# Performance work log

Measured on AMD Instinct MI355X. Metric: run time of the kernel, lower is better.

The kernel has to match this reference:

```python
import jax, jax.numpy as jnp
import numpy as np

B, P, N, D = 32, 100, 1000, 128
SQRT_D = 11.313708498984761
CLIP = 10.0


def setup_inputs() -> dict:
    key = jax.random.key(0)
    ks = jax.random.split(key, 8)
    s = 1.0 / np.sqrt(D)  # keep k ~ N(0,1) so exp(k) is stable
    return {
        "encoded_nodes": jax.random.normal(ks[0], (B, N, D), jnp.float32),
        "encoded_q1": jax.random.normal(ks[1], (B, P, D), jnp.float32),
        "encoded_last_node": jax.random.normal(ks[2], (B, P, D), jnp.float32),
        "cur_dist": jax.random.uniform(ks[3], (B, P, N), jnp.float32),
        "ninf_mask": jnp.zeros((B, P, N), jnp.float32),
        "log_scale": jnp.ones((1,), jnp.float32),
        "Wq_first": jax.random.normal(ks[4], (D, D), jnp.float32) * s,
        "Wq_last": jax.random.normal(ks[5], (D, D), jnp.float32) * s,
        "Wk": jax.random.normal(ks[6], (D, D), jnp.float32) * s,
        "Wv": jax.random.normal(ks[7], (D, D), jnp.float32) * s,
        "dist_alpha_1": jnp.ones((1,), jnp.float32),
        "AFT_dist_alpha_1": jnp.ones((1,), jnp.float32),
    }


def reference(encoded_nodes, encoded_q1, encoded_last_node, cur_dist, ninf_mask,
              log_scale, Wq_first, Wq_last, Wk, Wv, dist_alpha_1, AFT_dist_alpha_1):
    # set_kv / set_q1 (torch Linear: x @ W.T)
    k = jnp.einsum('bnd,ed->bne', encoded_nodes, Wk)          # [B,N,D]
    v = jnp.einsum('bnd,ed->bne', encoded_nodes, Wv)          # [B,N,D]
    q_first = jnp.einsum('bpd,ed->bpe', encoded_q1, Wq_first) # [B,P,D]
    q_last = jnp.einsum('bpd,ed->bpe', encoded_last_node, Wq_last)
    q = q_first + q_last

    cur_dist_out = -cur_dist                                   # [B,P,N]
    bias_scale = log_scale * AFT_dist_alpha_1 * cur_dist_out + ninf_mask
    ebias = jnp.exp(bias_scale)                                # [B,P,N]
    ek = jnp.exp(k)                                            # [B,N,D]
    num = jnp.einsum('bpn,bnd->bpd', ebias, ek * v)
    den = jnp.einsum('bpn,bnd->bpd', ebias, ek)
    aft_out = jax.nn.sigmoid(q) * (num / den)                  # [B,P,D]

    score = jnp.einsum('bpd,bnd->bpn', aft_out, encoded_nodes) / SQRT_D
    score = score + log_scale * dist_alpha_1 * cur_dist_out
    score = CLIP * jnp.tanh(score) + ninf_mask
    return jax.nn.softmax(score, axis=2)
```

## Files before the change

### kernel.cpp

```cpp
#include <hip/hip_runtime.h>
#include <hip/hip_bf16.h>
#include <math.h>

#define B 32
#define P 100
#define N 1000
#define D 128

constexpr float SQRT_D_INV = 1.0f / 11.313708498984761f;
constexpr float CLIPV = 10.0f;

__device__ __forceinline__ void fma4(float4& a, float s, const float4& b) {
    a.x = fmaf(s, b.x, a.x);
    a.y = fmaf(s, b.y, a.y);
    a.z = fmaf(s, b.z, a.z);
    a.w = fmaf(s, b.w, a.w);
}

__global__ void transpose_w4(const float* __restrict__ Wk,
                             const float* __restrict__ Wv,
                             const float* __restrict__ Wqf,
                             const float* __restrict__ Wql,
                             float* __restrict__ wkT,
                             float* __restrict__ wvT,
                             float* __restrict__ wqfT,
                             float* __restrict__ wqlT) {
    const int e = blockIdx.x;
    const int d = threadIdx.x;
    wkT[e * D + d]  = Wk[d * D + e];
    wvT[e * D + d]  = Wv[d * D + e];
    wqfT[e * D + d] = Wqf[d * D + e];
    wqlT[e * D + d] = Wql[d * D + e];
}

#define TT 64
__global__ __launch_bounds__(256) void transpose_nodes(
        const float* __restrict__ nodes, float* __restrict__ nodesT) {
    __shared__ float sh[TT][D + 1];
    const int ntiles = (N + TT - 1) / TT;
    const int b  = blockIdx.x / ntiles;
    const int n0 = (blockIdx.x % ntiles) * TT;
    const int t = threadIdx.x;
    const int rows = min(TT, N - n0);

    const float4* src = (const float4*)(nodes + ((long)b * N + n0) * D);
    for (int i = t; i < rows * (D / 4); i += 256) {
        int r = i >> 5, c = i & 31;
        float4 v = src[(long)r * (D / 4) + c];
        sh[r][c * 4 + 0] = v.x; sh[r][c * 4 + 1] = v.y;
        sh[r][c * 4 + 2] = v.z; sh[r][c * 4 + 3] = v.w;
    }
    __syncthreads();

    const int nl = t & 63;
    const int eg = t >> 6;
    if (nl < rows) {
        #pragma unroll
        for (int k = 0; k < 32; ++k) {
            int e = eg * 32 + k;
            nodesT[((long)b * D + e) * N + n0 + nl] = sh[nl][e];
        }
    }
}

#define R1 32
__global__ __launch_bounds__(256, 2) void kv_kernel(
        const float* __restrict__ nodes,
        const float* __restrict__ wkT,
        const float* __restrict__ wvT,
        float* __restrict__ ek,
        float* __restrict__ ekv) {
    __shared__ float sh[R1][D];
    const int t = threadIdx.x;
    const int dq = t & 31;
    const int rl = t >> 5;
    const long row0 = (long)blockIdx.x * R1;

    const float4* src = (const float4*)(nodes + row0 * D);
    float4* dst = (float4*)(&sh[0][0]);
    #pragma unroll
    for (int i = 0; i < (R1 * D / 4) / 256; ++i)
        dst[t + i * 256] = src[t + i * 256];
    __syncthreads();

    float4 ka[4], va[4];
    #pragma unroll
    for (int rr = 0; rr < 4; ++rr) {
        ka[rr] = make_float4(0.f, 0.f, 0.f, 0.f);
        va[rr] = make_float4(0.f, 0.f, 0.f, 0.f);
    }

    const float* wkp = wkT + dq * 4;
    const float* wvp = wvT + dq * 4;
    #pragma unroll 4
    for (int e0 = 0; e0 < D; e0 += 4) {
        float4 wk4[4], wv4[4];
        #pragma unroll
        for (int ee = 0; ee < 4; ++ee) {
            wk4[ee] = *(const float4*)(wkp + (e0 + ee) * D);
            wv4[ee] = *(const float4*)(wvp + (e0 + ee) * D);
        }
        #pragma unroll
        for (int rr = 0; rr < 4; ++rr) {
            float4 s4 = *(const float4*)(&sh[rl * 4 + rr][e0]);
            fma4(ka[rr], s4.x, wk4[0]); fma4(ka[rr], s4.y, wk4[1]);
            fma4(ka[rr], s4.z, wk4[2]); fma4(ka[rr], s4.w, wk4[3]);
            fma4(va[rr], s4.x, wv4[0]); fma4(va[rr], s4.y, wv4[1]);
            fma4(va[rr], s4.z, wv4[2]); fma4(va[rr], s4.w, wv4[3]);
        }
    }

    #pragma unroll
    for (int rr = 0; rr < 4; ++rr) {
        long row = row0 + rl * 4 + rr;
        float4 e4;
        e4.x = __expf(ka[rr].x); e4.y = __expf(ka[rr].y);
        e4.z = __expf(ka[rr].z); e4.w = __expf(ka[rr].w);
        float4 ev;
        ev.x = e4.x * va[rr].x; ev.y = e4.y * va[rr].y;
        ev.z = e4.z * va[rr].z; ev.w = e4.w * va[rr].w;
        *(float4*)(ek + row * D + dq * 4) = e4;
        *(float4*)(ekv + row * D + dq * 4) = ev;
    }
}

#define R2 16
__global__ __launch_bounds__(256, 2) void q_kernel(
        const float* __restrict__ q1,
        const float* __restrict__ qlast,
        const float* __restrict__ wqfT,
        const float* __restrict__ wqlT,
        float* __restrict__ qsig) {
    __shared__ float sh1[R2][D];
    __shared__ float sh2[R2][D];
    const int t = threadIdx.x;
    const int dq = t & 31;
    const int rl = t >> 5;
    const long row0 = (long)blockIdx.x * R2;

    const float4* s1 = (const float4*)(q1 + row0 * D);
    const float4* s2 = (const float4*)(qlast + row0 * D);
    float4* d1 = (float4*)(&sh1[0][0]);
    float4* d2 = (float4*)(&sh2[0][0]);
    #pragma unroll
    for (int i = 0; i < (R2 * D / 4) / 256; ++i) {
        d1[t + i * 256] = s1[t + i * 256];
        d2[t + i * 256] = s2[t + i * 256];
    }
    __syncthreads();

    float4 acc[2];
    acc[0] = make_float4(0.f, 0.f, 0.f, 0.f);
    acc[1] = make_float4(0.f, 0.f, 0.f, 0.f);

    const float* wfp = wqfT + dq * 4;
    const float* wlp = wqlT + dq * 4;
    #pragma unroll 4
    for (int e0 = 0; e0 < D; e0 += 4) {
        float4 wf4[4], wl4[4];
        #pragma unroll
        for (int ee = 0; ee < 4; ++ee) {
            wf4[ee] = *(const float4*)(wfp + (e0 + ee) * D);
            wl4[ee] = *(const float4*)(wlp + (e0 + ee) * D);
        }
        #pragma unroll
        for (int rr = 0; rr < 2; ++rr) {
            float4 a4 = *(const float4*)(&sh1[rl * 2 + rr][e0]);
            float4 b4 = *(const float4*)(&sh2[rl * 2 + rr][e0]);
            fma4(acc[rr], a4.x, wf4[0]); fma4(acc[rr], a4.y, wf4[1]);
            fma4(acc[rr], a4.z, wf4[2]); fma4(acc[rr], a4.w, wf4[3]);
            fma4(acc[rr], b4.x, wl4[0]); fma4(acc[rr], b4.y, wl4[1]);
            fma4(acc[rr], b4.z, wl4[2]); fma4(acc[rr], b4.w, wl4[3]);
        }
    }

    #pragma unroll
    for (int rr = 0; rr < 2; ++rr) {
        long row = row0 + rl * 2 + rr;
        float4 s;
        s.x = 1.0f / (1.0f + __expf(-acc[rr].x));
        s.y = 1.0f / (1.0f + __expf(-acc[rr].y));
        s.z = 1.0f / (1.0f + __expf(-acc[rr].z));
        s.w = 1.0f / (1.0f + __expf(-acc[rr].w));
        *(float4*)(qsig + row * D + dq * 4) = s;
    }
}

#define PT 20
__global__ __launch_bounds__(128, 2) void aft_part_kernel(
        const float* __restrict__ cur_dist,
        const float* __restrict__ ninf,
        const float* __restrict__ ek,
        const float* __restrict__ ekv,
        const float* __restrict__ log_scale,
        const float* __restrict__ aft_alpha,
        float* __restrict__ pnum,
        float* __restrict__ pden,
        int NC, int L) {
    __shared__ float eb[128][PT];
    const int t = threadIdx.x;
    const int dq = t & 31;
    const int pl = t >> 5;
    const int c  = blockIdx.x % NC;
    const int pt = (blockIdx.x / NC) % (P / PT);
    const int b  = blockIdx.x / (NC * (P / PT));
    const int p0 = pt * PT;
    const int n_begin = c * L;
    const int n_end = min(N, n_begin + L);
    const float lsA = log_scale[0] * aft_alpha[0];

    float4 num[5], den[5];
    #pragma unroll
    for (int i = 0; i < 5; ++i) {
        num[i] = make_float4(0.f, 0.f, 0.f, 0.f);
        den[i] = make_float4(0.f, 0.f, 0.f, 0.f);
    }

    for (int n0 = n_begin; n0 < n_end; n0 += 128) {
        const int lim = min(128, n_end - n0);
        __syncthreads();
        if (t < lim) {
            int n = n0 + t;
            #pragma unroll
            for (int i = 0; i < PT; ++i) {
                long idx = ((long)b * P + p0 + i) * N + n;
                eb[t][i] = __expf(fmaf(-lsA, cur_dist[idx], ninf[idx]));
            }
        }
        __syncthreads();
        #pragma unroll 4
        for (int j = 0; j < lim; ++j) {
            long base = ((long)b * N + n0 + j) * D + dq * 4;
            float4 ekq = *(const float4*)(ek + base);
            float4 evq = *(const float4*)(ekv + base);
            float4 e4 = *(const float4*)(&eb[j][pl * 4]);
            float es = eb[j][16 + pl];
            fma4(num[0], e4.x, evq); fma4(den[0], e4.x, ekq);
            fma4(num[1], e4.y, evq); fma4(den[1], e4.y, ekq);
            fma4(num[2], e4.z, evq); fma4(den[2], e4.z, ekq);
            fma4(num[3], e4.w, evq); fma4(den[3], e4.w, ekq);
            fma4(num[4], es,   evq); fma4(den[4], es,   ekq);
        }
    }

    #pragma unroll
    for (int r = 0; r < 4; ++r) {
        int p = pl * 4 + r;
        long o = (((long)c * B + b) * P + p0 + p) * D + dq * 4;
        *(float4*)(pnum + o) = num[r];
        *(float4*)(pden + o) = den[r];
    }
    {
        int p = 16 + pl;
        long o = (((long)c * B + b) * P + p0 + p) * D + dq * 4;
        *(float4*)(pnum + o) = num[4];
        *(float4*)(pden + o) = den[4];
    }
}

__global__ void aft_reduce_kernel(const float* __restrict__ pnum,
                                  const float* __restrict__ pden,
                                  const float* __restrict__ qsig,
                                  float* __restrict__ aft,
                                  int NC) {
    const long i = (long)blockIdx.x * 256 + threadIdx.x;
    const long BPD = (long)B * P * D;
    float n = 0.f, d = 0.f;
    for (int c = 0; c < NC; ++c) {
        n += pnum[(long)c * BPD + i];
        d += pden[(long)c * BPD + i];
    }
    aft[i] = qsig[i] * n / d;
}

#define PT2 10
__global__ __launch_bounds__(512) void score_kernel(
        const float* __restrict__ aft,
        const float* __restrict__ nodesT,
        const float* __restrict__ cur_dist,
        const float* __restrict__ ninf,
        const float* __restrict__ log_scale,
        const float* __restrict__ dist_alpha,
        float* __restrict__ out) {
    __shared__ float sa[PT2][D];
    __shared__ float red[8][PT2];
    __shared__ float bmax[PT2];
    __shared__ float bsum[PT2];
    const int t = threadIdx.x;
    const int wid = t >> 6;
    const int pt = blockIdx.x % (P / PT2);
    const int b  = blockIdx.x / (P / PT2);
    const int p0 = pt * PT2;
    const float lsA = log_scale[0] * dist_alpha[0];

    {
        const float4* src = (const float4*)(aft + ((long)b * P + p0) * D);
        float4* dst = (float4*)(&sa[0][0]);
        if (t < PT2 * D / 4) dst[t] = src[t];
    }
    __syncthreads();

    const int n0 = t * 2;
    const bool act = (n0 < N);
    const int ncl = act ? n0 : 0;
    const float* ntb = nodesT + (long)b * D * N;

    float2 acc[PT2];
    #pragma unroll
    for (int i = 0; i < PT2; ++i) acc[i] = make_float2(0.f, 0.f);

    #pragma unroll 4
    for (int e0 = 0; e0 < D; e0 += 4) {
        float2 x[4];
        #pragma unroll
        for (int ee = 0; ee < 4; ++ee)
            x[ee] = *(const float2*)(ntb + (long)(e0 + ee) * N + ncl);
        #pragma unroll
        for (int i = 0; i < PT2; ++i) {
            float4 a4 = *(const float4*)(&sa[i][e0]);
            acc[i].x = fmaf(x[0].x, a4.x, acc[i].x);
            acc[i].x = fmaf(x[1].x, a4.y, acc[i].x);
            acc[i].x = fmaf(x[2].x, a4.z, acc[i].x);
            acc[i].x = fmaf(x[3].x, a4.w, acc[i].x);
            acc[i].y = fmaf(x[0].y, a4.x, acc[i].y);
            acc[i].y = fmaf(x[1].y, a4.y, acc[i].y);
            acc[i].y = fmaf(x[2].y, a4.z, acc[i].y);
            acc[i].y = fmaf(x[3].y, a4.w, acc[i].y);
        }
    }

    float2 sc[PT2];
    #pragma unroll
    for (int i = 0; i < PT2; ++i) {
        if (act) {
            long idx = ((long)b * P + p0 + i) * N + n0;
            float2 cd = *(const float2*)(cur_dist + idx);
            float2 nf = *(const float2*)(ninf + idx);
            float sx = fmaf(acc[i].x, SQRT_D_INV, -lsA * cd.x);
            float sy = fmaf(acc[i].y, SQRT_D_INV, -lsA * cd.y);
            float ax = fabsf(sx), ay = fabsf(sy);
            float rx = 1.f - 2.f / (__expf(2.f * ax) + 1.f);
            float ry = 1.f - 2.f / (__expf(2.f * ay) + 1.f);
            sc[i].x = CLIPV * copysignf(rx, sx) + nf.x;
            sc[i].y = CLIPV * copysignf(ry, sy) + nf.y;
        } else {
            sc[i].x = -INFINITY;
            sc[i].y = -INFINITY;
        }
    }

    #pragma unroll
    for (int i = 0; i < PT2; ++i) {
        float m = fmaxf(sc[i].x, sc[i].y);
        #pragma unroll
        for (int o = 1; o < 64; o <<= 1) m = fmaxf(m, __shfl_xor(m, o, 64));
        if ((t & 63) == 0) red[wid][i] = m;
    }
    __syncthreads();
    if (t < PT2) {
        float mm = red[0][t];
        #pragma unroll
        for (int w = 1; w < 8; ++w) mm = fmaxf(mm, red[w][t]);
        bmax[t] = mm;
    }
    __syncthreads();

    float2 ex[PT2];
    #pragma unroll
    for (int i = 0; i < PT2; ++i) {
        float m = bmax[i];
        ex[i].x = (sc[i].x > -1e30f) ? __expf(sc[i].x - m) : 0.f;
        ex[i].y = (sc[i].y > -1e30f) ? __expf(sc[i].y - m) : 0.f;
        float ssum = ex[i].x + ex[i].y;
        #pragma unroll
        for (int o = 1; o < 64; o <<= 1) ssum += __shfl_xor(ssum, o, 64);
        if ((t & 63) == 0) red[wid][i] = ssum;
    }
    __syncthreads();
    if (t < PT2) {
        float ss = red[0][t];
        #pragma unroll
        for (int w = 1; w < 8; ++w) ss += red[w][t];
        bsum[t] = ss;
    }
    __syncthreads();

    #pragma unroll
    for (int i = 0; i < PT2; ++i) {
        if (act) {
            float inv = 1.0f / bsum[i];
            long idx = ((long)b * P + p0 + i) * N + n0;
            *(float2*)(out + idx) = make_float2(ex[i].x * inv, ex[i].y * inv);
        }
    }
}

extern "C" void kernel_launch(void* const* d_in, const int* in_sizes, int n_in,
                              void* d_out, int out_size, void* d_ws, size_t ws_size,
                              hipStream_t stream) {
    const float* nodes      = (const float*)d_in[0];
    const float* q1         = (const float*)d_in[1];
    const float* qlast      = (const float*)d_in[2];
    const float* cur_dist   = (const float*)d_in[3];
    const float* ninf       = (const float*)d_in[4];
    const float* log_scale  = (const float*)d_in[5];
    const float* Wqf        = (const float*)d_in[6];
    const float* Wql        = (const float*)d_in[7];
    const float* Wk         = (const float*)d_in[8];
    const float* Wv         = (const float*)d_in[9];
    const float* dist_alpha = (const float*)d_in[10];
    const float* aft_alpha  = (const float*)d_in[11];
    float* out = (float*)d_out;

    const long BND = (long)B * N * D;
    const long BPD = (long)B * P * D;
    const long W2  = (long)D * D;

    float* ws     = (float*)d_ws;
    float* ek     = ws;
    float* ekv    = ek + BND;
    float* qsig   = ekv + BND;
    float* aft    = qsig + BPD;
    float* wkT    = aft + BPD;
    float* wvT    = wkT + W2;
    float* wqfT   = wvT + W2;
    float* wqlT   = wqfT + W2;
    float* nodesT = wqlT + W2;
    float* pnum   = nodesT + BND;

    long avail = (long)(ws_size / 4) - (3 * BND + 2 * BPD + 4 * W2);
    int NC = (int)(avail / (2 * BPD));
    if (NC < 1) NC = 1;
    if (NC > 16) NC = 16;
    int L = (N + NC - 1) / NC;
    float* pden = pnum + (long)NC * BPD;

    transpose_w4<<<D, D, 0, stream>>>(Wk, Wv, Wqf, Wql, wkT, wvT, wqfT, wqlT);
    transpose_nodes<<<B * ((N + TT - 1) / TT), 256, 0, stream>>>(nodes, nodesT);
    kv_kernel<<<(B * N) / R1, 256, 0, stream>>>(nodes, wkT, wvT, ek, ekv);
    q_kernel<<<(B * P) / R2, 256, 0, stream>>>(q1, qlast, wqfT, wqlT, qsig);
    aft_part_kernel<<<B * (P / PT) * NC, 128, 0, stream>>>(
        cur_dist, ninf, ek, ekv, log_scale, aft_alpha, pnum, pden, NC, L);
    aft_reduce_kernel<<<(int)(BPD / 256), 256, 0, stream>>>(pnum, pden, qsig, aft, NC);
    score_kernel<<<B * (P / PT2), 512, 0, stream>>>(
        aft, nodesT, cur_dist, ninf, log_scale, dist_alpha, out);
}
```

Baseline: 257.9 us.

## Widen AFT partial tile to 50 queries and fuse reduction into score kernel

The AFT partial kernel now processes 50 query rows per block with 320 threads (10 warps of 5 rows each). This halves how many times the ek/ekv rows are re-read per batch, and a padded shared buffer avoids bank conflicts. The separate partial-sum reduction kernel is removed: the score kernel now sums the NC partials and applies the sigmoid gate while loading its query tile, saving one launch and one intermediate buffer. The chunk count is capped at 12 instead of 16, which gives fewer blocks and less parallelism, and the score kernel's prologue does more global reads.

Result: slower. 286.0 us (+10.9%).

```diff
diff --git a/kernel.cpp b/kernel.cpp
--- a/kernel.cpp
+++ b/kernel.cpp
@@ -186,8 +186,9 @@
     }
 }
 
-#define PT 20
-__global__ __launch_bounds__(128, 2) void aft_part_kernel(
+#define PT 50
+#define EBS 51
+__global__ __launch_bounds__(320, 4) void aft_part_kernel(
         const float* __restrict__ cur_dist,
         const float* __restrict__ ninf,
         const float* __restrict__ ek,
@@ -197,7 +198,7 @@
         float* __restrict__ pnum,
         float* __restrict__ pden,
         int NC, int L) {
-    __shared__ float eb[128][PT];
+    __shared__ float eb[128 * EBS];
     const int t = threadIdx.x;
     const int dq = t & 31;
     const int pl = t >> 5;
@@ -219,12 +220,12 @@
     for (int n0 = n_begin; n0 < n_end; n0 += 128) {
         const int lim = min(128, n_end - n0);
         __syncthreads();
-        if (t < lim) {
-            int n = n0 + t;
-            #pragma unroll
-            for (int i = 0; i < PT; ++i) {
-                long idx = ((long)b * P + p0 + i) * N + n;
-                eb[t][i] = __expf(fmaf(-lsA, cur_dist[idx], ninf[idx]));
+        for (int s = t; s < PT * 128; s += 320) {
+            int nl = s & 127;
+            int pp = s >> 7;
+            if (nl < lim) {
+                long idx = ((long)b * P + p0 + pp) * N + (n0 + nl);
+                eb[nl * EBS + pp] = __expf(fmaf(-lsA, cur_dist[idx], ninf[idx]));
             }
         }
         __syncthreads();
@@ -233,55 +234,36 @@
             long base = ((long)b * N + n0 + j) * D + dq * 4;
             float4 ekq = *(const float4*)(ek + base);
             float4 evq = *(const float4*)(ekv + base);
-            float4 e4 = *(const float4*)(&eb[j][pl * 4]);
-            float es = eb[j][16 + pl];
-            fma4(num[0], e4.x, evq); fma4(den[0], e4.x, ekq);
-            fma4(num[1], e4.y, evq); fma4(den[1], e4.y, ekq);
-            fma4(num[2], e4.z, evq); fma4(den[2], e4.z, ekq);
-            fma4(num[3], e4.w, evq); fma4(den[3], e4.w, ekq);
-            fma4(num[4], es,   evq); fma4(den[4], es,   ekq);
-        }
-    }
-
-    #pragma unroll
-    for (int r = 0; r < 4; ++r) {
-        int p = pl * 4 + r;
-        long o = (((long)c * B + b) * P + p0 + p) * D + dq * 4;
+            const float* ebp = &eb[j * EBS + pl * 5];
+            #pragma unroll
+            for (int r = 0; r < 5; ++r) {
+                float e = ebp[r];
+                fma4(num[r], e, evq);
+                fma4(den[r], e, ekq);
+            }
+        }
+    }
+
+    #pragma unroll
+    for (int r = 0; r < 5; ++r) {
+        int p = p0 + pl * 5 + r;
+        long o = (((long)c * B + b) * P + p) * D + dq * 4;
         *(float4*)(pnum + o) = num[r];
         *(float4*)(pden + o) = den[r];
     }
-    {
-        int p = 16 + pl;
-        long o = (((long)c * B + b) * P + p0 + p) * D + dq * 4;
-        *(float4*)(pnum + o) = num[4];
-        *(float4*)(pden + o) = den[4];
-    }
-}
-
-__global__ void aft_reduce_kernel(const float* __restrict__ pnum,
-                                  const float* __restrict__ pden,
-                                  const float* __restrict__ qsig,
-                                  float* __restrict__ aft,
-                                  int NC) {
-    const long i = (long)blockIdx.x * 256 + threadIdx.x;
-    const long BPD = (long)B * P * D;
-    float n = 0.f, d = 0.f;
-    for (int c = 0; c < NC; ++c) {
-        n += pnum[(long)c * BPD + i];
-        d += pden[(long)c * BPD + i];
-    }
-    aft[i] = qsig[i] * n / d;
 }
 
 #define PT2 10
 __global__ __launch_bounds__(512) void score_kernel(
-        const float* __restrict__ aft,
+        const float* __restrict__ pnum,
+        const float* __restrict__ pden,
+        const float* __restrict__ qsig,
         const float* __restrict__ nodesT,
         const float* __restrict__ cur_dist,
         const float* __restrict__ ninf,
         const float* __restrict__ log_scale,
         const float* __restrict__ dist_alpha,
-        float* __restrict__ out) {
+        float* __restrict__ out, int NC) {
     __shared__ float sa[PT2][D];
     __shared__ float red[8][PT2];
     __shared__ float bmax[PT2];
@@ -292,11 +274,18 @@
     const int b  = blockIdx.x / (P / PT2);
     const int p0 = pt * PT2;
     const float lsA = log_scale[0] * dist_alpha[0];
-
-    {
-        const float4* src = (const float4*)(aft + ((long)b * P + p0) * D);
-        float4* dst = (float4*)(&sa[0][0]);
-        if (t < PT2 * D / 4) dst[t] = src[t];
+    const long BPD = (long)B * P * D;
+
+    for (int idx = t; idx < PT2 * D; idx += 512) {
+        int i = idx >> 7;
+        int d = idx & 127;
+        long o = ((long)b * P + p0 + i) * D + d;
+        float nsum = 0.f, dsum = 0.f;
+        for (int c = 0; c < NC; ++c) {
+            nsum += pnum[(long)c * BPD + o];
+            dsum += pden[(long)c * BPD + o];
+        }
+        sa[i][d] = qsig[o] * nsum / dsum;
     }
     __syncthreads();
 
@@ -420,18 +409,17 @@
     float* ek     = ws;
     float* ekv    = ek + BND;
     float* qsig   = ekv + BND;
-    float* aft    = qsig + BPD;
-    float* wkT    = aft + BPD;
+    float* wkT    = qsig + BPD;
     float* wvT    = wkT + W2;
     float* wqfT   = wvT + W2;
     float* wqlT   = wqfT + W2;
     float* nodesT = wqlT + W2;
     float* pnum   = nodesT + BND;
 
-    long avail = (long)(ws_size / 4) - (3 * BND + 2 * BPD + 4 * W2);
+    long avail = (long)(ws_size / 4) - (3 * BND + BPD + 4 * W2);
     int NC = (int)(avail / (2 * BPD));
     if (NC < 1) NC = 1;
-    if (NC > 16) NC = 16;
+    if (NC > 12) NC = 12;
     int L = (N + NC - 1) / NC;
     float* pden = pnum + (long)NC * BPD;
 
@@ -439,9 +427,8 @@
     transpose_nodes<<<B * ((N + TT - 1) / TT), 256, 0, stream>>>(nodes, nodesT);
     kv_kernel<<<(B * N) / R1, 256, 0, stream>>>(nodes, wkT, wvT, ek, ekv);
     q_kernel<<<(B * P) / R2, 256, 0, stream>>>(q1, qlast, wqfT, wqlT, qsig);
-    aft_part_kernel<<<B * (P / PT) * NC, 128, 0, stream>>>(
+    aft_part_kernel<<<B * (P / PT) * NC, 320, 0, stream>>>(
         cur_dist, ninf, ek, ekv, log_scale, aft_alpha, pnum, pden, NC, L);
-    aft_reduce_kernel<<<(int)(BPD / 256), 256, 0, stream>>>(pnum, pden, qsig, aft, NC);
     score_kernel<<<B * (P / PT2), 512, 0, stream>>>(
-        aft, nodesT, cur_dist, ninf, log_scale, dist_alpha, out);
-}
+        pnum, pden, qsig, nodesT, cur_dist, ninf, log_scale, dist_alpha, out, NC);
+}
```

## Register-prefetch operand loads in all GEMM loops and fuse AFT reduction into score

Applied to the files above, without the earlier changes.

Adds software double-buffering in registers to the kv, q, aft_part and score kernels: the next iteration's weight or ek/ekv/nodesT operands are loaded while the current FMAs run. The separate aft_reduce kernel is removed; score_kernel now sums the partial num/den across chunks and applies the sigmoid gate while filling its shared tile. This saves one launch and one round trip of the aft buffer through memory. The chunk length is rounded up to a multiple of 4 to fit the unrolled-by-4 loop, and the min-blocks launch bound is dropped, which may raise register use and lower occupancy.

Measured after the change: 258.8 us. No clear change (+0.4%).

```diff
diff --git a/kernel.cpp b/kernel.cpp
--- a/kernel.cpp
+++ b/kernel.cpp
@@ -64,7 +64,7 @@
 }
 
 #define R1 32
-__global__ __launch_bounds__(256, 2) void kv_kernel(
+__global__ __launch_bounds__(256) void kv_kernel(
         const float* __restrict__ nodes,
         const float* __restrict__ wkT,
         const float* __restrict__ wvT,
@@ -92,22 +92,33 @@
 
     const float* wkp = wkT + dq * 4;
     const float* wvp = wvT + dq * 4;
-    #pragma unroll 4
+
+    float4 cwk[4], cwv[4];
+    #pragma unroll
+    for (int ee = 0; ee < 4; ++ee) {
+        cwk[ee] = *(const float4*)(wkp + ee * D);
+        cwv[ee] = *(const float4*)(wvp + ee * D);
+    }
+
     for (int e0 = 0; e0 < D; e0 += 4) {
-        float4 wk4[4], wv4[4];
-        #pragma unroll
-        for (int ee = 0; ee < 4; ++ee) {
-            wk4[ee] = *(const float4*)(wkp + (e0 + ee) * D);
-            wv4[ee] = *(const float4*)(wvp + (e0 + ee) * D);
+        float4 nwk[4], nwv[4];
+        if (e0 + 4 < D) {
+            #pragma unroll
+            for (int ee = 0; ee < 4; ++ee) {
+                nwk[ee] = *(const float4*)(wkp + (e0 + 4 + ee) * D);
+                nwv[ee] = *(const float4*)(wvp + (e0 + 4 + ee) * D);
+            }
         }
         #pragma unroll
         for (int rr = 0; rr < 4; ++rr) {
             float4 s4 = *(const float4*)(&sh[rl * 4 + rr][e0]);
-            fma4(ka[rr], s4.x, wk4[0]); fma4(ka[rr], s4.y, wk4[1]);
-            fma4(ka[rr], s4.z, wk4[2]); fma4(ka[rr], s4.w, wk4[3]);
-            fma4(va[rr], s4.x, wv4[0]); fma4(va[rr], s4.y, wv4[1]);
-            fma4(va[rr], s4.z, wv4[2]); fma4(va[rr], s4.w, wv4[3]);
-        }
+            fma4(ka[rr], s4.x, cwk[0]); fma4(ka[rr], s4.y, cwk[1]);
+            fma4(ka[rr], s4.z, cwk[2]); fma4(ka[rr], s4.w, cwk[3]);
+            fma4(va[rr], s4.x, cwv[0]); fma4(va[rr], s4.y, cwv[1]);
+            fma4(va[rr], s4.z, cwv[2]); fma4(va[rr], s4.w, cwv[3]);
+        }
+        #pragma unroll
+        for (int ee = 0; ee < 4; ++ee) { cwk[ee] = nwk[ee]; cwv[ee] = nwv[ee]; }
     }
 
     #pragma unroll
@@ -125,7 +136,7 @@
 }
 
 #define R2 16
-__global__ __launch_bounds__(256, 2) void q_kernel(
+__global__ __launch_bounds__(256) void q_kernel(
         const float* __restrict__ q1,
         const float* __restrict__ qlast,
         const float* __restrict__ wqfT,
@@ -155,23 +166,34 @@
 
     const float* wfp = wqfT + dq * 4;
     const float* wlp = wqlT + dq * 4;
-    #pragma unroll 4
+
+    float4 cwf[4], cwl[4];
+    #pragma unroll
+    for (int ee = 0; ee < 4; ++ee) {
+        cwf[ee] = *(const float4*)(wfp + ee * D);
+        cwl[ee] = *(const float4*)(wlp + ee * D);
+    }
+
     for (int e0 = 0; e0 < D; e0 += 4) {
-        float4 wf4[4], wl4[4];
-        #pragma unroll
-        for (int ee = 0; ee < 4; ++ee) {
-            wf4[ee] = *(const float4*)(wfp + (e0 + ee) * D);
-            wl4[ee] = *(const float4*)(wlp + (e0 + ee) * D);
+        float4 nwf[4], nwl[4];
+        if (e0 + 4 < D) {
+            #pragma unroll
+            for (int ee = 0; ee < 4; ++ee) {
+                nwf[ee] = *(const float4*)(wfp + (e0 + 4 + ee) * D);
+                nwl[ee] = *(const float4*)(wlp + (e0 + 4 + ee) * D);
+            }
         }
         #pragma unroll
         for (int rr = 0; rr < 2; ++rr) {
             float4 a4 = *(const float4*)(&sh1[rl * 2 + rr][e0]);
             float4 b4 = *(const float4*)(&sh2[rl * 2 + rr][e0]);
-            fma4(acc[rr], a4.x, wf4[0]); fma4(acc[rr], a4.y, wf4[1]);
-            fma4(acc[rr], a4.z, wf4[2]); fma4(acc[rr], a4.w, wf4[3]);
-            fma4(acc[rr], b4.x, wl4[0]); fma4(acc[rr], b4.y, wl4[1]);
-            fma4(acc[rr], b4.z, wl4[2]); fma4(acc[rr], b4.w, wl4[3]);
-        }
+            fma4(acc[rr], a4.x, cwf[0]); fma4(acc[rr], a4.y, cwf[1]);
+            fma4(acc[rr], a4.z, cwf[2]); fma4(acc[rr], a4.w, cwf[3]);
+            fma4(acc[rr], b4.x, cwl[0]); fma4(acc[rr], b4.y, cwl[1]);
+            fma4(acc[rr], b4.z, cwl[2]); fma4(acc[rr], b4.w, cwl[3]);
+        }
+        #pragma unroll
+        for (int ee = 0; ee < 4; ++ee) { cwf[ee] = nwf[ee]; cwl[ee] = nwl[ee]; }
     }
 
     #pragma unroll
@@ -187,7 +209,7 @@
 }
 
 #define PT 20
-__global__ __launch_bounds__(128, 2) void aft_part_kernel(
+__global__ __launch_bounds__(128) void aft_part_kernel(
         const float* __restrict__ cur_dist,
         const float* __restrict__ ninf,
         const float* __restrict__ ek,
@@ -228,18 +250,39 @@
             }
         }
         __syncthreads();
-        #pragma unroll 4
-        for (int j = 0; j < lim; ++j) {
-            long base = ((long)b * N + n0 + j) * D + dq * 4;
-            float4 ekq = *(const float4*)(ek + base);
-            float4 evq = *(const float4*)(ekv + base);
-            float4 e4 = *(const float4*)(&eb[j][pl * 4]);
-            float es = eb[j][16 + pl];
-            fma4(num[0], e4.x, evq); fma4(den[0], e4.x, ekq);
-            fma4(num[1], e4.y, evq); fma4(den[1], e4.y, ekq);
-            fma4(num[2], e4.z, evq); fma4(den[2], e4.z, ekq);
-            fma4(num[3], e4.w, evq); fma4(den[3], e4.w, ekq);
-            fma4(num[4], es,   evq); fma4(den[4], es,   ekq);
+
+        const float* ekb = ek  + ((long)b * N + n0) * D + dq * 4;
+        const float* evb = ekv + ((long)b * N + n0) * D + dq * 4;
+
+        float4 cek[4], cev[4];
+        #pragma unroll
+        for (int jj = 0; jj < 4; ++jj) {
+            cek[jj] = *(const float4*)(ekb + (long)jj * D);
+            cev[jj] = *(const float4*)(evb + (long)jj * D);
+        }
+
+        for (int jb = 0; jb < lim; jb += 4) {
+            float4 nek[4], nev[4];
+            if (jb + 4 < lim) {
+                #pragma unroll
+                for (int jj = 0; jj < 4; ++jj) {
+                    nek[jj] = *(const float4*)(ekb + (long)(jb + 4 + jj) * D);
+                    nev[jj] = *(const float4*)(evb + (long)(jb + 4 + jj) * D);
+                }
+            }
+            #pragma unroll
+            for (int jj = 0; jj < 4; ++jj) {
+                const int j = jb + jj;
+                float4 e4 = *(const float4*)(&eb[j][pl * 4]);
+                float es = eb[j][16 + pl];
+                fma4(num[0], e4.x, cev[jj]); fma4(den[0], e4.x, cek[jj]);
+                fma4(num[1], e4.y, cev[jj]); fma4(den[1], e4.y, cek[jj]);
+                fma4(num[2], e4.z, cev[jj]); fma4(den[2], e4.z, cek[jj]);
+                fma4(num[3], e4.w, cev[jj]); fma4(den[3], e4.w, cek[jj]);
+                fma4(num[4], es,   cev[jj]); fma4(den[4], es,   cek[jj]);
+            }
+            #pragma unroll
+            for (int jj = 0; jj < 4; ++jj) { cek[jj] = nek[jj]; cev[jj] = nev[jj]; }
         }
     }
 
@@ -258,30 +301,17 @@
     }
 }
 
-__global__ void aft_reduce_kernel(const float* __restrict__ pnum,
-                                  const float* __restrict__ pden,
-                                  const float* __restrict__ qsig,
-                                  float* __restrict__ aft,
-                                  int NC) {
-    const long i = (long)blockIdx.x * 256 + threadIdx.x;
-    const long BPD = (long)B * P * D;
-    float n = 0.f, d = 0.f;
-    for (int c = 0; c < NC; ++c) {
-        n += pnum[(long)c * BPD + i];
-        d += pden[(long)c * BPD + i];
-    }
-    aft[i] = qsig[i] * n / d;
-}
-
 #define PT2 10
 __global__ __launch_bounds__(512) void score_kernel(
-        const float* __restrict__ aft,
+        const float* __restrict__ pnum,
+        const float* __restrict__ pden,
+        const float* __restrict__ qsig,
         const float* __restrict__ nodesT,
         const float* __restrict__ cur_dist,
         const float* __restrict__ ninf,
         const float* __restrict__ log_scale,
         const float* __restrict__ dist_alpha,
-        float* __restrict__ out) {
+        float* __restrict__ out, int NC) {
     __shared__ float sa[PT2][D];
     __shared__ float red[8][PT2];
     __shared__ float bmax[PT2];
@@ -292,11 +322,18 @@
     const int b  = blockIdx.x / (P / PT2);
     const int p0 = pt * PT2;
     const float lsA = log_scale[0] * dist_alpha[0];
-
-    {
-        const float4* src = (const float4*)(aft + ((long)b * P + p0) * D);
-        float4* dst = (float4*)(&sa[0][0]);
-        if (t < PT2 * D / 4) dst[t] = src[t];
+    const long BPD = (long)B * P * D;
+
+    for (int idx = t; idx < PT2 * D; idx += 512) {
+        int i = idx >> 7;
+        int d = idx & 127;
+        long o = ((long)b * P + p0 + i) * D + d;
+        float nsum = 0.f, dsum = 0.f;
+        for (int c = 0; c < NC; ++c) {
+            nsum += pnum[(long)c * BPD + o];
+            dsum += pden[(long)c * BPD + o];
+        }
+        sa[i][d] = qsig[o] * nsum / dsum;
     }
     __syncthreads();
 
@@ -309,24 +346,32 @@
     #pragma unroll
     for (int i = 0; i < PT2; ++i) acc[i] = make_float2(0.f, 0.f);
 
-    #pragma unroll 4
+    float2 cx[4];
+    #pragma unroll
+    for (int ee = 0; ee < 4; ++ee)
+        cx[ee] = *(const float2*)(ntb + (long)ee * N + ncl);
+
     for (int e0 = 0; e0 < D; e0 += 4) {
-        float2 x[4];
-        #pragma unroll
-        for (int ee = 0; ee < 4; ++ee)
-            x[ee] = *(const float2*)(ntb + (long)(e0 + ee) * N + ncl);
+        float2 nx[4];
+        if (e0 + 4 < D) {
+            #pragma unroll
+            for (int ee = 0; ee < 4; ++ee)
+                nx[ee] = *(const float2*)(ntb + (long)(e0 + 4 + ee) * N + ncl);
+        }
         #pragma unroll
         for (int i = 0; i < PT2; ++i) {
             float4 a4 = *(const float4*)(&sa[i][e0]);
-            acc[i].x = fmaf(x[0].x, a4.x, acc[i].x);
-            acc[i].x = fmaf(x[1].x, a4.y, acc[i].x);
-            acc[i].x = fmaf(x[2].x, a4.z, acc[i].x);
-            acc[i].x = fmaf(x[3].x, a4.w, acc[i].x);
-            acc[i].y = fmaf(x[0].y, a4.x, acc[i].y);
-            acc[i].y = fmaf(x[1].y, a4.y, acc[i].y);
-            acc[i].y = fmaf(x[2].y, a4.z, acc[i].y);
-            acc[i].y = fmaf(x[3].y, a4.w, acc[i].y);
-        }
+            acc[i].x = fmaf(cx[0].x, a4.x, acc[i].x);
+            acc[i].x = fmaf(cx[1].x, a4.y, acc[i].x);
+            acc[i].x = fmaf(cx[2].x, a4.z, acc[i].x);
+            acc[i].x = fmaf(cx[3].x, a4.w, acc[i].x);
+            acc[i].y = fmaf(cx[0].y, a4.x, acc[i].y);
+            acc[i].y = fmaf(cx[1].y, a4.y, acc[i].y);
+            acc[i].y = fmaf(cx[2].y, a4.z, acc[i].y);
+            acc[i].y = fmaf(cx[3].y, a4.w, acc[i].y);
+        }
+        #pragma unroll
+        for (int ee = 0; ee < 4; ++ee) cx[ee] = nx[ee];
     }
 
     float2 sc[PT2];
@@ -420,19 +465,19 @@
     float* ek     = ws;
     float* ekv    = ek + BND;
     float* qsig   = ekv + BND;
-    float* aft    = qsig + BPD;
-    float* wkT    = aft + BPD;
+    float* wkT    = qsig + BPD;
     float* wvT    = wkT + W2;
     float* wqfT   = wvT + W2;
     float* wqlT   = wqfT + W2;
     float* nodesT = wqlT + W2;
     float* pnum   = nodesT + BND;
 
-    long avail = (long)(ws_size / 4) - (3 * BND + 2 * BPD + 4 * W2);
+    long avail = (long)(ws_size / 4) - (3 * BND + BPD + 4 * W2);
     int NC = (int)(avail / (2 * BPD));
     if (NC < 1) NC = 1;
     if (NC > 16) NC = 16;
-    int L = (N + NC - 1) / NC;
+    int L = (((N + NC - 1) / NC) + 3) & ~3;
+    NC = (N + L - 1) / L;
     float* pden = pnum + (long)NC * BPD;
 
     transpose_w4<<<D, D, 0, stream>>>(Wk, Wv, Wqf, Wql, wkT, wvT, wqfT, wqlT);
@@ -441,7 +486,6 @@
     q_kernel<<<(B * P) / R2, 256, 0, stream>>>(q1, qlast, wqfT, wqlT, qsig);
     aft_part_kernel<<<B * (P / PT) * NC, 128, 0, stream>>>(
         cur_dist, ninf, ek, ekv, log_scale, aft_alpha, pnum, pden, NC, L);
-    aft_reduce_kernel<<<(int)(BPD / 256), 256, 0, stream>>>(pnum, pden, qsig, aft, NC);
     score_kernel<<<B * (P / PT2), 512, 0, stream>>>(
-        aft, nodesT, cur_dist, ninf, log_scale, dist_alpha, out);
-}
+        pnum, pden, qsig, nodesT, cur_dist, ninf, log_scale, dist_alpha, out, NC);
+}
```
